# Optimization experiments

Measured on AMD Instinct MI355X. Metric: run time of the kernel, lower is better.

## Reference

```python
import jax, jax.numpy as jnp
import numpy as np

N, L = 131072, 4          # traffic lights, lanes per TL
E, H = 64, 128            # embed_dim, hidden_dim
NH, HD = 4, 16            # num_heads, head_dim (E = NH*HD)
NR, R = 4, 8              # num_regions, region_embed_dim
INIT_LOG_STD = -0.5


def _lin(k, fan_in, shape):
    b = 1.0 / np.sqrt(fan_in)
    return jax.random.uniform(k, shape, minval=-b, maxval=b, dtype=jnp.float32)


def setup_inputs() -> dict:
    key = jax.random.key(0)
    ks = jax.random.split(key, 32)
    inp = {
        "queue": jax.random.uniform(ks[0], (N, L), dtype=jnp.float32),
        "waiting": jax.random.uniform(ks[1], (N, L), dtype=jnp.float32),
        "phase_onehot": jax.random.uniform(ks[2], (N, 4), dtype=jnp.float32),
        "elapsed": jax.random.uniform(ks[3], (N,), dtype=jnp.float32),
        "region_ids": jax.random.randint(ks[4], (N,), 0, NR, dtype=jnp.int32),
        "noise": jax.random.normal(ks[5], (N,), dtype=jnp.float32),
        # lane_mlp: Linear(3,H) -> ReLU -> Linear(H,E) -> ReLU
        "lane_w1": _lin(ks[6], 3, (3, H)), "lane_b1": _lin(ks[7], 3, (H,)),
        "lane_w2": _lin(ks[8], H, (H, E)), "lane_b2": _lin(ks[9], H, (E,)),
        # MultiheadAttention in/out projections
        "attn_in_w": _lin(ks[10], E, (E, 3 * E)), "attn_in_b": jnp.zeros((3 * E,), jnp.float32),
        "attn_out_w": _lin(ks[11], E, (E, E)), "attn_out_b": jnp.zeros((E,), jnp.float32),
        # phase_mlp: Linear(5,H) -> ReLU -> Linear(H,H) -> ReLU
        "phase_w1": _lin(ks[12], 5, (5, H)), "phase_b1": _lin(ks[13], 5, (H,)),
        "phase_w2": _lin(ks[14], H, (H, H)), "phase_b2": _lin(ks[15], H, (H,)),
        # region embedding table
        "region_table": jax.random.normal(ks[16], (NR, R), dtype=jnp.float32),
        # mlp_head: Linear(E+H+R, H) -> ReLU -> Linear(H, 1)
        "head_w1": _lin(ks[17], E + H + R, (E + H + R, H)), "head_b1": _lin(ks[18], E + H + R, (H,)),
        "head_w2": _lin(ks[19], H, (H, 1)), "head_b2": _lin(ks[20], H, (1,)),
        "log_std": jnp.full((1,), INIT_LOG_STD, dtype=jnp.float32),
    }
    return inp


def reference(queue, waiting, phase_onehot, elapsed, region_ids, noise,
              lane_w1, lane_b1, lane_w2, lane_b2,
              attn_in_w, attn_in_b, attn_out_w, attn_out_b,
              phase_w1, phase_b1, phase_w2, phase_b2,
              region_table, head_w1, head_b1, head_w2, head_b2, log_std):
    # --- lane context: tiny MLP + self-attention over L lanes, batched over N TLs ---
    lane_feats = jnp.stack([queue, waiting, jnp.broadcast_to(elapsed[:, None], (N, L))], axis=-1)  # [N,L,3]
    h = jax.nn.relu(lane_feats @ lane_w1 + lane_b1)          # [N,L,H]
    emb = jax.nn.relu(h @ lane_w2 + lane_b2)                 # [N,L,E]

    qkv = emb @ attn_in_w + attn_in_b                        # [N,L,3E]
    q, k, v = jnp.split(qkv, 3, axis=-1)
    def heads(x):  # [N,L,E] -> [N,NH,L,HD]
        return x.reshape(N, L, NH, HD).transpose(0, 2, 1, 3)
    q, k, v = heads(q), heads(k), heads(v)
    scores = jnp.einsum('bhqd,bhkd->bhqk', q, k) / np.sqrt(HD)   # [N,NH,L,L]
    attn = jax.nn.softmax(scores, axis=-1)
    o = jnp.einsum('bhqk,bhkd->bhqd', attn, v)               # [N,NH,L,HD]
    o = o.transpose(0, 2, 1, 3).reshape(N, L, E)
    attn_out = o @ attn_out_w + attn_out_b                   # [N,L,E]
    ctx = attn_out.mean(axis=1)                              # [N,E]

    # --- phase MLP ---
    phase_elapsed = jnp.concatenate([phase_onehot, elapsed[:, None]], axis=-1)  # [N,5]
    ph = jax.nn.relu(phase_elapsed @ phase_w1 + phase_b1)
    phase_emb = jax.nn.relu(ph @ phase_w2 + phase_b2)        # [N,H]

    # --- region embedding (clamped index) ---
    rid = jnp.clip(region_ids, 0, NR - 1)
    region_emb = region_table[rid]                           # [N,R]

    # --- Gaussian head ---
    feat = jnp.concatenate([ctx, phase_emb, region_emb], axis=-1)  # [N,E+H+R]
    means = (jax.nn.relu(feat @ head_w1 + head_b1) @ head_w2 + head_b2)[:, 0]  # [N]

    ls = jnp.broadcast_to(log_std, means.shape)
    std = jnp.exp(ls)
    actions = means + std * noise
    actions_clamped = jnp.clip(actions, -1.0, 1.0)
    log_prob = -0.5 * ((actions - means) ** 2 / (std * std) + 2.0 * ls + np.log(2.0 * np.pi))
    return actions_clamped, log_prob
```

## Files before the change

### kernel.cpp

```cpp
#include <hip/hip_runtime.h>
#include <math.h>

#define N_TL 131072
#define GRID 2048
#define BLK 256

typedef __attribute__((ext_vector_type(8))) short bfrag;
typedef __attribute__((ext_vector_type(4))) float f32x4;

__device__ __forceinline__ unsigned short f2bf_rne(float x) {
  unsigned int u = __float_as_uint(x);
  return (unsigned short)((u + 0x7fffu + ((u >> 16) & 1u)) >> 16);
}
__device__ __forceinline__ unsigned int pack2(float a, float b) {
  return __builtin_amdgcn_perm(__float_as_uint(b) + 0x8000u,
                               __float_as_uint(a) + 0x8000u, 0x07060302u);
}
__device__ __forceinline__ float lo16(unsigned int u) { return __uint_as_float(u << 16); }
__device__ __forceinline__ float hi16(unsigned int u) { return __uint_as_float(u & 0xffff0000u); }
__device__ __forceinline__ f32x4 mfma16(bfrag a, bfrag b, f32x4 c) {
  return __builtin_amdgcn_mfma_f32_16x16x32_bf16(a, b, c, 0, 0, 0);
}

__device__ __forceinline__ bfrag load_wfragT(const float* __restrict__ w, int ncols,
                                             int col0, int k0, int lane, int K, float scale) {
  const int mm = lane & 15, qq = lane >> 4;
  bfrag f;
  #pragma unroll
  for (int j = 0; j < 8; ++j) {
    const int k = k0 + qq * 8 + j;
    const float v = (k < K) ? w[(size_t)k * ncols + col0 + mm] * scale : 0.f;
    f[j] = (short)f2bf_rne(v);
  }
  return f;
}

#define LDBACT(arr, stride, nt, kk) \
  (*reinterpret_cast<const bfrag*>(&(arr)[((nt) * 16 + m) * (stride) + (kk) * 32 + quad * 8]))

struct alignas(16) SmemF {
  union {
    unsigned short qkv[64 * 200];
    unsigned short h[64 * 136];
    unsigned short ph[64 * 136];
  };
  unsigned short emb[64 * 72];
  unsigned short xbuf[64 * 32];
  unsigned short feat[64 * 200];
  float b1[128], b2[64], bin[192], bout[64];
  float pb1[128], pb2[128];
  float rbias[4][128];
  float hw2[128];
  float consts[2];
  int ridx[64];
};

__global__ __launch_bounds__(BLK, 2)
void fused_policy(const float* __restrict__ queue,
                  const float* __restrict__ waiting,
                  const float* __restrict__ phase_onehot,
                  const float* __restrict__ elapsed,
                  const int* __restrict__ region_ids,
                  const float* __restrict__ noise,
                  const float* __restrict__ lane_w1,
                  const float* __restrict__ lane_b1,
                  const float* __restrict__ lane_w2,
                  const float* __restrict__ lane_b2,
                  const float* __restrict__ attn_in_w,
                  const float* __restrict__ attn_in_b,
                  const float* __restrict__ attn_out_w,
                  const float* __restrict__ attn_out_b,
                  const float* __restrict__ phase_w1,
                  const float* __restrict__ phase_b1,
                  const float* __restrict__ phase_w2,
                  const float* __restrict__ phase_b2,
                  const float* __restrict__ region_table,
                  const float* __restrict__ head_w1,
                  const float* __restrict__ head_b1,
                  const float* __restrict__ head_w2,
                  const float* __restrict__ head_b2,
                  const float* __restrict__ log_std,
                  float* __restrict__ out) {
  __shared__ SmemF S;
  const int tid  = threadIdx.x;
  const int wv   = tid >> 6;
  const int lane = tid & 63;
  const int m    = lane & 15;
  const int quad = lane >> 4;
  const int n0   = blockIdx.x * 64;

  bfrag wL1[2], wL2[4], wQKV[3][2], wOUT2[2];
  #pragma unroll
  for (int Mi = 0; Mi < 2; ++Mi)
    wL1[Mi] = load_wfragT(lane_w1, 128, (wv * 2 + Mi) * 16, 0, lane, 3, 1.f);
  #pragma unroll
  for (int kk = 0; kk < 4; ++kk)
    wL2[kk] = load_wfragT(lane_w2, 64, wv * 16, kk * 32, lane, 128, 1.f);
  #pragma unroll
  for (int Mi = 0; Mi < 3; ++Mi)
    #pragma unroll
    for (int kk = 0; kk < 2; ++kk)
      wQKV[Mi][kk] = load_wfragT(attn_in_w, 192, (wv + Mi * 4) * 16, kk * 32, lane, 64,
                                 Mi == 0 ? 0.25f : 1.f);
  #pragma unroll
  for (int kk = 0; kk < 2; ++kk) {
    bfrag f;
    #pragma unroll
    for (int j = 0; j < 8; ++j) {
      const int k = kk * 32 + quad * 8 + j;
      f[j] = (short)f2bf_rne(attn_out_w[(size_t)k * 64 + wv * 16 + m] * 0.25f);
    }
    wOUT2[kk] = f;
  }

  for (int i = tid; i < 128; i += BLK) S.b1[i] = lane_b1[i];
  for (int i = tid; i < 64;  i += BLK) S.b2[i] = lane_b2[i];
  for (int i = tid; i < 192; i += BLK) S.bin[i] = attn_in_b[i] * ((i < 64) ? 0.25f : 1.f);
  for (int i = tid; i < 64;  i += BLK) S.bout[i] = attn_out_b[i];
  for (int i = tid; i < 128; i += BLK) S.pb1[i] = phase_b1[i];
  for (int i = tid; i < 128; i += BLK) S.pb2[i] = phase_b2[i];
  for (int i = tid; i < 128; i += BLK) S.hw2[i] = head_w2[i];
  for (int i = tid; i < 512; i += BLK) {
    const int g = i >> 7, c = i & 127;
    float acc = head_b1[c];
    #pragma unroll
    for (int j = 0; j < 8; ++j) acc += region_table[g * 8 + j] * head_w1[(192 + j) * 128 + c];
    S.rbias[g][c] = acc;
  }
  if (tid == 0) { S.consts[0] = head_b2[0]; S.consts[1] = log_std[0]; }
  if (tid < 64) {
    int r = region_ids[n0 + tid];
    S.ridx[tid] = r < 0 ? 0 : (r > 3 ? 3 : r);
  }
  {
    const int r = tid >> 2, seg = tid & 3;
    uint4 z = {0, 0, 0, 0};
    if (seg == 0) {
      const int gl = n0 * 4 + r;
      z.x = pack2(queue[gl], waiting[gl]);
      z.y = pack2(elapsed[n0 + (r >> 2)], 0.f);
    }
    *reinterpret_cast<uint4*>(&S.xbuf[r * 32 + seg * 8]) = z;
  }
  __syncthreads();

  #pragma unroll 1
  for (int s = 0; s < 4; ++s) {
    const int tl0 = n0 + s * 16;

    {
      f32x4 acc[2][4];
      #pragma unroll
      for (int Mi = 0; Mi < 2; ++Mi) {
        const f32x4 bb = *reinterpret_cast<const f32x4*>(&S.b1[(wv * 2 + Mi) * 16 + quad * 4]);
        #pragma unroll
        for (int Nt = 0; Nt < 4; ++Nt) acc[Mi][Nt] = bb;
      }
      #pragma unroll
      for (int Nt = 0; Nt < 4; ++Nt) {
        const bfrag b = LDBACT(S.xbuf, 32, Nt, 0);
        acc[0][Nt] = mfma16(wL1[0], b, acc[0][Nt]);
        acc[1][Nt] = mfma16(wL1[1], b, acc[1][Nt]);
      }
      #pragma unroll
      for (int Mi = 0; Mi < 2; ++Mi) {
        const int oc0 = (wv * 2 + Mi) * 16 + quad * 4;
        #pragma unroll
        for (int Nt = 0; Nt < 4; ++Nt) {
          const int row = Nt * 16 + m;
          uint2 u;
          u.x = pack2(fmaxf(acc[Mi][Nt][0], 0.f), fmaxf(acc[Mi][Nt][1], 0.f));
          u.y = pack2(fmaxf(acc[Mi][Nt][2], 0.f), fmaxf(acc[Mi][Nt][3], 0.f));
          *reinterpret_cast<uint2*>(&S.h[row * 136 + oc0]) = u;
        }
      }
    }
    __syncthreads();

    {
      const int oc0 = wv * 16 + quad * 4;
      const f32x4 bb = *reinterpret_cast<const f32x4*>(&S.b2[oc0]);
      f32x4 acc[4] = {bb, bb, bb, bb};
      #pragma unroll
      for (int Nt = 0; Nt < 4; ++Nt)
        #pragma unroll
        for (int kk = 0; kk < 4; ++kk)
          acc[Nt] = mfma16(wL2[kk], LDBACT(S.h, 136, Nt, kk), acc[Nt]);
      #pragma unroll
      for (int Nt = 0; Nt < 4; ++Nt) {
        const int row = Nt * 16 + m;
        uint2 u;
        u.x = pack2(fmaxf(acc[Nt][0], 0.f), fmaxf(acc[Nt][1], 0.f));
        u.y = pack2(fmaxf(acc[Nt][2], 0.f), fmaxf(acc[Nt][3], 0.f));
        *reinterpret_cast<uint2*>(&S.emb[row * 72 + oc0]) = u;
      }
    }
    __syncthreads();

    {
      f32x4 acc[3][4];
      #pragma unroll
      for (int Mi = 0; Mi < 3; ++Mi) {
        const f32x4 bb = *reinterpret_cast<const f32x4*>(&S.bin[(wv + Mi * 4) * 16 + quad * 4]);
        #pragma unroll
        for (int Nt = 0; Nt < 4; ++Nt) acc[Mi][Nt] = bb;
      }
      #pragma unroll
      for (int Nt = 0; Nt < 4; ++Nt) {
        const bfrag e0 = LDBACT(S.emb, 72, Nt, 0);
        const bfrag e1 = LDBACT(S.emb, 72, Nt, 1);
        #pragma unroll
        for (int Mi = 0; Mi < 3; ++Mi) {
          acc[Mi][Nt] = mfma16(wQKV[Mi][0], e0, acc[Mi][Nt]);
          acc[Mi][Nt] = mfma16(wQKV[Mi][1], e1, acc[Mi][Nt]);
        }
      }
      #pragma unroll
      for (int Mi = 0; Mi < 3; ++Mi) {
        const int oc0 = (wv + Mi * 4) * 16 + quad * 4;
        #pragma unroll
        for (int Nt = 0; Nt < 4; ++Nt) {
          const int row = Nt * 16 + m;
          uint2 u;
          u.x = pack2(acc[Mi][Nt][0], acc[Mi][Nt][1]);
          u.y = pack2(acc[Mi][Nt][2], acc[Mi][Nt][3]);
          *reinterpret_cast<uint2*>(&S.qkv[row * 200 + oc0]) = u;
        }
      }
      const int r = tid >> 2, seg = tid & 3;
      uint4 z = {0, 0, 0, 0};
      if (s < 3) {
        if (seg == 0) {
          const int gl = (tl0 + 16) * 4 + r;
          z.x = pack2(queue[gl], waiting[gl]);
          z.y = pack2(elapsed[tl0 + 16 + (r >> 2)], 0.f);
        }
      } else {
        if (seg == 0) {
          const float4 p = *reinterpret_cast<const float4*>(&phase_onehot[(n0 + r) * 4]);
          z.x = pack2(p.x, p.y);
          z.y = pack2(p.z, p.w);
          z.z = pack2(elapsed[n0 + r], 0.f);
        }
      }
      *reinterpret_cast<uint4*>(&S.xbuf[r * 32 + seg * 8]) = z;
    }
    __syncthreads();

    {
      const int tl = tid >> 4, l16 = tid & 15;
      const int hh = l16 >> 2, lq = l16 & 3;
      const unsigned int* qp = reinterpret_cast<const unsigned int*>(
          &S.qkv[(tl * 4 + lq) * 200 + hh * 16]);
      unsigned int qu[8];
      #pragma unroll
      for (int j = 0; j < 8; ++j) qu[j] = qp[j];
      float qlo[8], qhi[8];
      #pragma unroll
      for (int j = 0; j < 8; ++j) { qlo[j] = lo16(qu[j]); qhi[j] = hi16(qu[j]); }
      float sc[4];
      #pragma unroll
      for (int lk = 0; lk < 4; ++lk) {
        const unsigned int* kp = reinterpret_cast<const unsigned int*>(
            &S.qkv[(tl * 4 + lk) * 200 + 64 + hh * 16]);
        float tx = 0.f, ty = 0.f;
        #pragma unroll
        for (int j = 0; j < 8; ++j) {
          const unsigned int ku = kp[j];
          tx += qlo[j] * lo16(ku);
          ty += qhi[j] * hi16(ku);
        }
        sc[lk] = tx + ty;
      }
      const float mx = fmaxf(fmaxf(sc[0], sc[1]), fmaxf(sc[2], sc[3]));
      const float e0 = __expf(sc[0] - mx), e1 = __expf(sc[1] - mx);
      const float e2 = __expf(sc[2] - mx), e3 = __expf(sc[3] - mx);
      const float inv = 1.f / (e0 + e1 + e2 + e3);
      const float pr[4] = {e0 * inv, e1 * inv, e2 * inv, e3 * inv};
      float olo[8], ohi[8];
      #pragma unroll
      for (int j = 0; j < 8; ++j) { olo[j] = 0.f; ohi[j] = 0.f; }
      #pragma unroll
      for (int lk = 0; lk < 4; ++lk) {
        const unsigned int* vp = reinterpret_cast<const unsigned int*>(
            &S.qkv[(tl * 4 + lk) * 200 + 128 + hh * 16]);
        const float p = pr[lk];
        #pragma unroll
        for (int j = 0; j < 8; ++j) {
          const unsigned int vu = vp[j];
          olo[j] += p * lo16(vu);
          ohi[j] += p * hi16(vu);
        }
      }
      unsigned short* om = S.emb;
      const int base = tl * 264 + lq * 64 + hh * 16;
      *reinterpret_cast<uint4*>(&om[base]) =
          make_uint4(pack2(olo[0], ohi[0]), pack2(olo[1], ohi[1]),
                     pack2(olo[2], ohi[2]), pack2(olo[3], ohi[3]));
      *reinterpret_cast<uint4*>(&om[base + 8]) =
          make_uint4(pack2(olo[4], ohi[4]), pack2(olo[5], ohi[5]),
                     pack2(olo[6], ohi[6]), pack2(olo[7], ohi[7]));
    }
    __syncthreads();

    {
      const int oc0 = wv * 16 + quad * 4;
      f32x4 acc = *reinterpret_cast<const f32x4*>(&S.bout[oc0]);
      #pragma unroll
      for (int kk = 0; kk < 8; ++kk)
        acc = mfma16(wOUT2[kk & 1], LDBACT(S.emb, 264, 0, kk), acc);
      uint2 u;
      u.x = pack2(acc[0], acc[1]);
      u.y = pack2(acc[2], acc[3]);
      *reinterpret_cast<uint2*>(&S.feat[(s * 16 + m) * 200 + oc0]) = u;
    }
  }
  __syncthreads();

  __builtin_amdgcn_sched_barrier(0);
  bfrag wP1[2], wP2[2][4], wH1[2][6];
  #pragma unroll
  for (int Mi = 0; Mi < 2; ++Mi) {
    wP1[Mi] = load_wfragT(phase_w1, 128, (wv * 2 + Mi) * 16, 0, lane, 5, 1.f);
    #pragma unroll
    for (int kk = 0; kk < 4; ++kk)
      wP2[Mi][kk] = load_wfragT(phase_w2, 128, (wv * 2 + Mi) * 16, kk * 32, lane, 128, 1.f);
    #pragma unroll
    for (int kk = 0; kk < 6; ++kk)
      wH1[Mi][kk] = load_wfragT(head_w1, 128, (wv * 2 + Mi) * 16, kk * 32, lane, 192, 1.f);
  }

  {
    f32x4 acc[2][4];
    #pragma unroll
    for (int Mi = 0; Mi < 2; ++Mi) {
      const f32x4 bb = *reinterpret_cast<const f32x4*>(&S.pb1[(wv * 2 + Mi) * 16 + quad * 4]);
      #pragma unroll
      for (int Nt = 0; Nt < 4; ++Nt) acc[Mi][Nt] = bb;
    }
    #pragma unroll
    for (int Nt = 0; Nt < 4; ++Nt) {
      const bfrag b = LDBACT(S.xbuf, 32, Nt, 0);
      acc[0][Nt] = mfma16(wP1[0], b, acc[0][Nt]);
      acc[1][Nt] = mfma16(wP1[1], b, acc[1][Nt]);
    }
    #pragma unroll
    for (int Mi = 0; Mi < 2; ++Mi) {
      const int oc0 = (wv * 2 + Mi) * 16 + quad * 4;
      #pragma unroll
      for (int Nt = 0; Nt < 4; ++Nt) {
        const int row = Nt * 16 + m;
        uint2 u;
        u.x = pack2(fmaxf(acc[Mi][Nt][0], 0.f), fmaxf(acc[Mi][Nt][1], 0.f));
        u.y = pack2(fmaxf(acc[Mi][Nt][2], 0.f), fmaxf(acc[Mi][Nt][3], 0.f));
        *reinterpret_cast<uint2*>(&S.ph[row * 136 + oc0]) = u;
      }
    }
  }
  __syncthreads();

  {
    f32x4 acc[2][4];
    #pragma unroll
    for (int Mi = 0; Mi < 2; ++Mi) {
      const f32x4 bb = *reinterpret_cast<const f32x4*>(&S.pb2[(wv * 2 + Mi) * 16 + quad * 4]);
      #pragma unroll
      for (int Nt = 0; Nt < 4; ++Nt) acc[Mi][Nt] = bb;
    }
    #pragma unroll
    for (int kk = 0; kk < 4; ++kk)
      #pragma unroll
      for (int Nt = 0; Nt < 4; ++Nt) {
        const bfrag b = LDBACT(S.ph, 136, Nt, kk);
        acc[0][Nt] = mfma16(wP2[0][kk], b, acc[0][Nt]);
        acc[1][Nt] = mfma16(wP2[1][kk], b, acc[1][Nt]);
      }
    #pragma unroll
    for (int Mi = 0; Mi < 2; ++Mi) {
      const int oc0 = (wv * 2 + Mi) * 16 + quad * 4;
      #pragma unroll
      for (int Nt = 0; Nt < 4; ++Nt) {
        const int row = Nt * 16 + m;
        uint2 u;
        u.x = pack2(fmaxf(acc[Mi][Nt][0], 0.f), fmaxf(acc[Mi][Nt][1], 0.f));
        u.y = pack2(fmaxf(acc[Mi][Nt][2], 0.f), fmaxf(acc[Mi][Nt][3], 0.f));
        *reinterpret_cast<uint2*>(&S.feat[row * 200 + 64 + oc0]) = u;
      }
    }
  }
  __syncthreads();

  {
    f32x4 acc[2][4];
    #pragma unroll
    for (int Mi = 0; Mi < 2; ++Mi) {
      const int oc0 = (wv * 2 + Mi) * 16 + quad * 4;
      #pragma unroll
      for (int Nt = 0; Nt < 4; ++Nt)
        acc[Mi][Nt] = *reinterpret_cast<const f32x4*>(&S.rbias[S.ridx[Nt * 16 + m]][oc0]);
    }
    #pragma unroll
    for (int kk = 0; kk < 6; ++kk)
      #pragma unroll
      for (int Nt = 0; Nt < 4; ++Nt) {
        const bfrag b = LDBACT(S.feat, 200, Nt, kk);
        acc[0][Nt] = mfma16(wH1[0][kk], b, acc[0][Nt]);
        acc[1][Nt] = mfma16(wH1[1][kk], b, acc[1][Nt]);
      }
    #pragma unroll
    for (int Mi = 0; Mi < 2; ++Mi) {
      const int oc0 = (wv * 2 + Mi) * 16 + quad * 4;
      #pragma unroll
      for (int Nt = 0; Nt < 4; ++Nt) {
        const int row = Nt * 16 + m;
        uint2 u;
        u.x = pack2(fmaxf(acc[Mi][Nt][0], 0.f), fmaxf(acc[Mi][Nt][1], 0.f));
        u.y = pack2(fmaxf(acc[Mi][Nt][2], 0.f), fmaxf(acc[Mi][Nt][3], 0.f));
        *reinterpret_cast<uint2*>(&S.ph[row * 136 + oc0]) = u;
      }
    }
  }
  __syncthreads();

  {
    const int tl = tid >> 2, s4 = tid & 3;
    const unsigned int* hp = reinterpret_cast<const unsigned int*>(&S.ph[tl * 136 + s4 * 32]);
    float t = 0.f;
    #pragma unroll
    for (int j = 0; j < 16; ++j) {
      const unsigned int hu = hp[j];
      t += lo16(hu) * S.hw2[s4 * 32 + 2 * j];
      t += hi16(hu) * S.hw2[s4 * 32 + 2 * j + 1];
    }
    t += __shfl_xor(t, 1);
    t += __shfl_xor(t, 2);
    if (s4 == 0) {
      const int n = n0 + tl;
      const float means = t + S.consts[0];
      const float ls = S.consts[1];
      const float nz = noise[n];
      const float a = means + __expf(ls) * nz;
      out[n] = fminf(fmaxf(a, -1.f), 1.f);
      out[N_TL + n] = -0.5f * (nz * nz + 2.f * ls + 1.8378770664093453f);
    }
  }
}

extern "C" void kernel_launch(void* const* d_in, const int* in_sizes, int n_in,
                              void* d_out, int out_size, void* d_ws, size_t ws_size,
                              hipStream_t stream) {
  const float* queue        = (const float*)d_in[0];
  const float* waiting      = (const float*)d_in[1];
  const float* phase_onehot = (const float*)d_in[2];
  const float* elapsed      = (const float*)d_in[3];
  const int*   region_ids   = (const int*)d_in[4];
  const float* noise        = (const float*)d_in[5];
  const float* lane_w1      = (const float*)d_in[6];
  const float* lane_b1      = (const float*)d_in[7];
  const float* lane_w2      = (const float*)d_in[8];
  const float* lane_b2      = (const float*)d_in[9];
  const float* attn_in_w    = (const float*)d_in[10];
  const float* attn_in_b    = (const float*)d_in[11];
  const float* attn_out_w   = (const float*)d_in[12];
  const float* attn_out_b   = (const float*)d_in[13];
  const float* phase_w1     = (const float*)d_in[14];
  const float* phase_b1     = (const float*)d_in[15];
  const float* phase_w2     = (const float*)d_in[16];
  const float* phase_b2     = (const float*)d_in[17];
  const float* region_table = (const float*)d_in[18];
  const float* head_w1      = (const float*)d_in[19];
  const float* head_b1      = (const float*)d_in[20];
  const float* head_w2      = (const float*)d_in[21];
  const float* head_b2      = (const float*)d_in[22];
  const float* log_std      = (const float*)d_in[23];

  float* out = (float*)d_out;
  (void)d_ws; (void)ws_size;

  hipLaunchKernelGGL(fused_policy, dim3(GRID), dim3(BLK), 0, stream,
                     queue, waiting, phase_onehot, elapsed, region_ids, noise,
                     lane_w1, lane_b1, lane_w2, lane_b2,
                     attn_in_w, attn_in_b, attn_out_w, attn_out_b,
                     phase_w1, phase_b1, phase_w2, phase_b2, region_table,
                     head_w1, head_b1, head_w2, head_b2, log_std, out);
}
```

Measured before the change: 200.5 us.

## Halve per-block tile to 32 lights, shrink LDS, raise occupancy to 3

```diff
diff --git a/kernel.cpp b/kernel.cpp
--- a/kernel.cpp
+++ b/kernel.cpp
@@ -2,7 +2,7 @@
 #include <math.h>
 
 #define N_TL 131072
-#define GRID 2048
+#define GRID 4096
 #define BLK 256
 
 typedef __attribute__((ext_vector_type(8))) short bfrag;
@@ -21,6 +21,9 @@
 __device__ __forceinline__ f32x4 mfma16(bfrag a, bfrag b, f32x4 c) {
   return __builtin_amdgcn_mfma_f32_16x16x32_bf16(a, b, c, 0, 0, 0);
 }
+__device__ __forceinline__ f32x4 ldg4(const float* __restrict__ p) {
+  return *reinterpret_cast<const f32x4*>(p);
+}
 
 __device__ __forceinline__ bfrag load_wfragT(const float* __restrict__ w, int ncols,
                                              int col0, int k0, int lane, int K, float scale) {
@@ -42,20 +45,16 @@
   union {
     unsigned short qkv[64 * 200];
     unsigned short h[64 * 136];
-    unsigned short ph[64 * 136];
+    unsigned short ph[32 * 136];
   };
   unsigned short emb[64 * 72];
   unsigned short xbuf[64 * 32];
-  unsigned short feat[64 * 200];
-  float b1[128], b2[64], bin[192], bout[64];
-  float pb1[128], pb2[128];
+  unsigned short feat[32 * 200];
   float rbias[4][128];
-  float hw2[128];
-  float consts[2];
-  int ridx[64];
+  int ridx[32];
 };
 
-__global__ __launch_bounds__(BLK, 2)
+__global__ __launch_bounds__(BLK, 3)
 void fused_policy(const float* __restrict__ queue,
                   const float* __restrict__ waiting,
                   const float* __restrict__ phase_onehot,
@@ -87,7 +86,7 @@
   const int lane = tid & 63;
   const int m    = lane & 15;
   const int quad = lane >> 4;
-  const int n0   = blockIdx.x * 64;
+  const int n0   = blockIdx.x * 32;
 
   bfrag wL1[2], wL2[4], wQKV[3][2], wOUT2[2];
   #pragma unroll
@@ -113,13 +112,6 @@
     wOUT2[kk] = f;
   }
 
-  for (int i = tid; i < 128; i += BLK) S.b1[i] = lane_b1[i];
-  for (int i = tid; i < 64;  i += BLK) S.b2[i] = lane_b2[i];
-  for (int i = tid; i < 192; i += BLK) S.bin[i] = attn_in_b[i] * ((i < 64) ? 0.25f : 1.f);
-  for (int i = tid; i < 64;  i += BLK) S.bout[i] = attn_out_b[i];
-  for (int i = tid; i < 128; i += BLK) S.pb1[i] = phase_b1[i];
-  for (int i = tid; i < 128; i += BLK) S.pb2[i] = phase_b2[i];
-  for (int i = tid; i < 128; i += BLK) S.hw2[i] = head_w2[i];
   for (int i = tid; i < 512; i += BLK) {
     const int g = i >> 7, c = i & 127;
     float acc = head_b1[c];
@@ -127,8 +119,7 @@
     for (int j = 0; j < 8; ++j) acc += region_table[g * 8 + j] * head_w1[(192 + j) * 128 + c];
     S.rbias[g][c] = acc;
   }
-  if (tid == 0) { S.consts[0] = head_b2[0]; S.consts[1] = log_std[0]; }
-  if (tid < 64) {
+  if (tid < 32) {
     int r = region_ids[n0 + tid];
     S.ridx[tid] = r < 0 ? 0 : (r > 3 ? 3 : r);
   }
@@ -145,14 +136,14 @@
   __syncthreads();
 
   #pragma unroll 1
-  for (int s = 0; s < 4; ++s) {
+  for (int s = 0; s < 2; ++s) {
     const int tl0 = n0 + s * 16;
 
     {
       f32x4 acc[2][4];
       #pragma unroll
       for (int Mi = 0; Mi < 2; ++Mi) {
-        const f32x4 bb = *reinterpret_cast<const f32x4*>(&S.b1[(wv * 2 + Mi) * 16 + quad * 4]);
+        const f32x4 bb = ldg4(&lane_b1[(wv * 2 + Mi) * 16 + quad * 4]);
         #pragma unroll
         for (int Nt = 0; Nt < 4; ++Nt) acc[Mi][Nt] = bb;
       }
@@ -179,7 +170,7 @@
 
     {
       const int oc0 = wv * 16 + quad * 4;
-      const f32x4 bb = *reinterpret_cast<const f32x4*>(&S.b2[oc0]);
+      const f32x4 bb = ldg4(&lane_b2[oc0]);
       f32x4 acc[4] = {bb, bb, bb, bb};
       #pragma unroll
       for (int Nt = 0; Nt < 4; ++Nt)
@@ -201,7 +192,8 @@
       f32x4 acc[3][4];
       #pragma unroll
       for (int Mi = 0; Mi < 3; ++Mi) {
-        const f32x4 bb = *reinterpret_cast<const f32x4*>(&S.bin[(wv + Mi * 4) * 16 + quad * 4]);
+        f32x4 bb = ldg4(&attn_in_b[(wv + Mi * 4) * 16 + quad * 4]);
+        if (Mi == 0) bb *= 0.25f;
         #pragma unroll
         for (int Nt = 0; Nt < 4; ++Nt) acc[Mi][Nt] = bb;
       }
@@ -229,14 +221,14 @@
       }
       const int r = tid >> 2, seg = tid & 3;
       uint4 z = {0, 0, 0, 0};
-      if (s < 3) {
+      if (s == 0) {
         if (seg == 0) {
           const int gl = (tl0 + 16) * 4 + r;
           z.x = pack2(queue[gl], waiting[gl]);
           z.y = pack2(elapsed[tl0 + 16 + (r >> 2)], 0.f);
         }
       } else {
-        if (seg == 0) {
+        if (seg == 0 && r < 32) {
           const float4 p = *reinterpret_cast<const float4*>(&phase_onehot[(n0 + r) * 4]);
           z.x = pack2(p.x, p.y);
           z.y = pack2(p.z, p.w);
@@ -305,7 +297,7 @@
 
     {
       const int oc0 = wv * 16 + quad * 4;
-      f32x4 acc = *reinterpret_cast<const f32x4*>(&S.bout[oc0]);
+      f32x4 acc = ldg4(&attn_out_b[oc0]);
       #pragma unroll
       for (int kk = 0; kk < 8; ++kk)
         acc = mfma16(wOUT2[kk & 1], LDBACT(S.emb, 264, 0, kk), acc);
@@ -331,15 +323,14 @@
   }
 
   {
-    f32x4 acc[2][4];
-    #pragma unroll
-    for (int Mi = 0; Mi < 2; ++Mi) {
-      const f32x4 bb = *reinterpret_cast<const f32x4*>(&S.pb1[(wv * 2 + Mi) * 16 + quad * 4]);
-      #pragma unroll
-      for (int Nt = 0; Nt < 4; ++Nt) acc[Mi][Nt] = bb;
-    }
-    #pragma unroll
-    for (int Nt = 0; Nt < 4; ++Nt) {
+    f32x4 acc[2][2];
+    #pragma unroll
+    for (int Mi = 0; Mi < 2; ++Mi) {
+      const f32x4 bb = ldg4(&phase_b1[(wv * 2 + Mi) * 16 + quad * 4]);
+      acc[Mi][0] = bb; acc[Mi][1] = bb;
+    }
+    #pragma unroll
+    for (int Nt = 0; Nt < 2; ++Nt) {
       const bfrag b = LDBACT(S.xbuf, 32, Nt, 0);
       acc[0][Nt] = mfma16(wP1[0], b, acc[0][Nt]);
       acc[1][Nt] = mfma16(wP1[1], b, acc[1][Nt]);
@@ -348,7 +339,7 @@
     for (int Mi = 0; Mi < 2; ++Mi) {
       const int oc0 = (wv * 2 + Mi) * 16 + quad * 4;
       #pragma unroll
-      for (int Nt = 0; Nt < 4; ++Nt) {
+      for (int Nt = 0; Nt < 2; ++Nt) {
         const int row = Nt * 16 + m;
         uint2 u;
         u.x = pack2(fmaxf(acc[Mi][Nt][0], 0.f), fmaxf(acc[Mi][Nt][1], 0.f));
@@ -360,17 +351,16 @@
   __syncthreads();
 
   {
-    f32x4 acc[2][4];
-    #pragma unroll
-    for (int Mi = 0; Mi < 2; ++Mi) {
-      const f32x4 bb = *reinterpret_cast<const f32x4*>(&S.pb2[(wv * 2 + Mi) * 16 + quad * 4]);
-      #pragma unroll
-      for (int Nt = 0; Nt < 4; ++Nt) acc[Mi][Nt] = bb;
+    f32x4 acc[2][2];
+    #pragma unroll
+    for (int Mi = 0; Mi < 2; ++Mi) {
+      const f32x4 bb = ldg4(&phase_b2[(wv * 2 + Mi) * 16 + quad * 4]);
+      acc[Mi][0] = bb; acc[Mi][1] = bb;
     }
     #pragma unroll
     for (int kk = 0; kk < 4; ++kk)
       #pragma unroll
-      for (int Nt = 0; Nt < 4; ++Nt) {
+      for (int Nt = 0; Nt < 2; ++Nt) {
         const bfrag b = LDBACT(S.ph, 136, Nt, kk);
         acc[0][Nt] = mfma16(wP2[0][kk], b, acc[0][Nt]);
         acc[1][Nt] = mfma16(wP2[1][kk], b, acc[1][Nt]);
@@ -379,7 +369,7 @@
     for (int Mi = 0; Mi < 2; ++Mi) {
       const int oc0 = (wv * 2 + Mi) * 16 + quad * 4;
       #pragma unroll
-      for (int Nt = 0; Nt < 4; ++Nt) {
+      for (int Nt = 0; Nt < 2; ++Nt) {
         const int row = Nt * 16 + m;
         uint2 u;
         u.x = pack2(fmaxf(acc[Mi][Nt][0], 0.f), fmaxf(acc[Mi][Nt][1], 0.f));
@@ -391,18 +381,18 @@
   __syncthreads();
 
   {
-    f32x4 acc[2][4];
+    f32x4 acc[2][2];
     #pragma unroll
     for (int Mi = 0; Mi < 2; ++Mi) {
       const int oc0 = (wv * 2 + Mi) * 16 + quad * 4;
       #pragma unroll
-      for (int Nt = 0; Nt < 4; ++Nt)
+      for (int Nt = 0; Nt < 2; ++Nt)
         acc[Mi][Nt] = *reinterpret_cast<const f32x4*>(&S.rbias[S.ridx[Nt * 16 + m]][oc0]);
     }
     #pragma unroll
     for (int kk = 0; kk < 6; ++kk)
       #pragma unroll
-      for (int Nt = 0; Nt < 4; ++Nt) {
+      for (int Nt = 0; Nt < 2; ++Nt) {
         const bfrag b = LDBACT(S.feat, 200, Nt, kk);
         acc[0][Nt] = mfma16(wH1[0][kk], b, acc[0][Nt]);
         acc[1][Nt] = mfma16(wH1[1][kk], b, acc[1][Nt]);
@@ -411,7 +401,7 @@
     for (int Mi = 0; Mi < 2; ++Mi) {
       const int oc0 = (wv * 2 + Mi) * 16 + quad * 4;
       #pragma unroll
-      for (int Nt = 0; Nt < 4; ++Nt) {
+      for (int Nt = 0; Nt < 2; ++Nt) {
         const int row = Nt * 16 + m;
         uint2 u;
         u.x = pack2(fmaxf(acc[Mi][Nt][0], 0.f), fmaxf(acc[Mi][Nt][1], 0.f));
@@ -423,21 +413,28 @@
   __syncthreads();
 
   {
-    const int tl = tid >> 2, s4 = tid & 3;
-    const unsigned int* hp = reinterpret_cast<const unsigned int*>(&S.ph[tl * 136 + s4 * 32]);
+    const int tl = tid >> 3, s8 = tid & 7;
+    const unsigned int* hp = reinterpret_cast<const unsigned int*>(&S.ph[tl * 136 + s8 * 16]);
+    const f32x4 w0 = ldg4(&head_w2[s8 * 16]);
+    const f32x4 w1 = ldg4(&head_w2[s8 * 16 + 4]);
+    const f32x4 w2 = ldg4(&head_w2[s8 * 16 + 8]);
+    const f32x4 w3 = ldg4(&head_w2[s8 * 16 + 12]);
+    float wreg[16] = {w0[0], w0[1], w0[2], w0[3], w1[0], w1[1], w1[2], w1[3],
+                      w2[0], w2[1], w2[2], w2[3], w3[0], w3[1], w3[2], w3[3]};
     float t = 0.f;
     #pragma unroll
-    for (int j = 0; j < 16; ++j) {
+    for (int j = 0; j < 8; ++j) {
       const unsigned int hu = hp[j];
-      t += lo16(hu) * S.hw2[s4 * 32 + 2 * j];
-      t += hi16(hu) * S.hw2[s4 * 32 + 2 * j + 1];
+      t += lo16(hu) * wreg[2 * j];
+      t += hi16(hu) * wreg[2 * j + 1];
     }
     t += __shfl_xor(t, 1);
     t += __shfl_xor(t, 2);
-    if (s4 == 0) {
+    t += __shfl_xor(t, 4);
+    if (s8 == 0) {
       const int n = n0 + tl;
-      const float means = t + S.consts[0];
-      const float ls = S.consts[1];
+      const float means = t + head_b2[0];
+      const float ls = log_std[0];
       const float nz = noise[n];
       const float a = means + __expf(ls) * nz;
       out[n] = fminf(fmaxf(a, -1.f), 1.f);
```

Measured after the change: 270.7 us. 1.35x slower.
